# Optimization experiments

Hardware: AMD Instinct MI355X
Metric: run time of the kernel (lower is better)

Reference implementation:

```python
import jax, jax.numpy as jnp
import numpy as np

COST_CLASS, COST_BBOX, COST_GIOU = 2.0, 5.0, 2.0
ALPHA, GAMMA, EPS = 0.25, 2.0, 1e-8


def _cxcywh_to_xyxy(b):
    cx, cy, w, h = b[..., 0], b[..., 1], b[..., 2], b[..., 3]
    return jnp.stack([cx - 0.5 * w, cy - 0.5 * h, cx + 0.5 * w, cy + 0.5 * h], axis=-1)


def _generalized_box_iou(boxes1, boxes2):
    # boxes1: [N,4], boxes2: [T,4] in xyxy -> [N,T]
    area1 = (boxes1[:, 2] - boxes1[:, 0]) * (boxes1[:, 3] - boxes1[:, 1])
    area2 = (boxes2[:, 2] - boxes2[:, 0]) * (boxes2[:, 3] - boxes2[:, 1])
    lt = jnp.maximum(boxes1[:, None, :2], boxes2[None, :, :2])
    rb = jnp.minimum(boxes1[:, None, 2:], boxes2[None, :, 2:])
    wh = jnp.clip(rb - lt, 0.0)
    inter = wh[..., 0] * wh[..., 1]
    union = area1[:, None] + area2[None, :] - inter
    iou = inter / union
    lt_e = jnp.minimum(boxes1[:, None, :2], boxes2[None, :, :2])
    rb_e = jnp.maximum(boxes1[:, None, 2:], boxes2[None, :, 2:])
    wh_e = jnp.clip(rb_e - lt_e, 0.0)
    area_e = wh_e[..., 0] * wh_e[..., 1]
    return iou - (area_e - union) / area_e


def setup_inputs() -> dict:
    key = jax.random.key(0)
    k1, k2, k3, k4 = jax.random.split(key, 4)
    bs, nq, nc, T = 16, 900, 91, 1600
    pred_logits = jax.random.normal(k1, (bs, nq, nc), dtype=jnp.float32)
    pred_boxes = jax.random.uniform(k2, (bs, nq, 4), dtype=jnp.float32)
    tgt_ids = jax.random.randint(k3, (T,), 0, nc, dtype=jnp.int64) if jax.config.jax_enable_x64 else jax.random.randint(k3, (T,), 0, nc, dtype=jnp.int32)
    tgt_bbox = jax.random.uniform(k4, (T, 4), dtype=jnp.float32)
    return {"pred_logits": pred_logits, "pred_boxes": pred_boxes,
            "tgt_ids": tgt_ids, "tgt_bbox": tgt_bbox}


def reference(pred_logits, pred_boxes, tgt_ids, tgt_bbox):
    bs, nq, nc = pred_logits.shape
    out_prob = jax.nn.sigmoid(pred_logits.reshape(bs * nq, nc))  # [N, C]
    out_bbox = pred_boxes.reshape(bs * nq, 4)                    # [N, 4]

    # -GIoU cost
    cost_giou = -_generalized_box_iou(_cxcywh_to_xyxy(out_bbox), _cxcywh_to_xyxy(tgt_bbox))

    # focal-style classification cost (alpha/gamma hardcoded in the source forward)
    neg_cost_class = (1.0 - ALPHA) * out_prob ** GAMMA * (-jnp.log(1.0 - out_prob + EPS))
    pos_cost_class = ALPHA * (1.0 - out_prob) ** GAMMA * (-jnp.log(out_prob + EPS))
    cost_class = pos_cost_class[:, tgt_ids] - neg_cost_class[:, tgt_ids]  # [N, T]

    # L1 cdist between box vectors
    cost_bbox = jnp.sum(jnp.abs(out_bbox[:, None, :] - tgt_bbox[None, :, :]), axis=-1)

    C = COST_BBOX * cost_bbox + COST_CLASS * cost_class + COST_GIOU * cost_giou
    return C.reshape(bs, nq, -1)
```

## Files before the change

### kernel.cpp

```cpp
#include <hip/hip_runtime.h>


#define NC 91
#define TT 1600
#define T4 (TT / 4)
#define ROWS 16
#define RPAD 20
#define NTHREADS 448
#define TABN (ROWS * NC)
#define TAB4 (TABN / 4)

typedef float vfloat4 __attribute__((ext_vector_type(4)));

__device__ __forceinline__ float focal_tab(float x) {
    const float p = __builtin_amdgcn_rcpf(1.f + __expf(-x));
    const float omp = 1.f - p;
    const float neg = 0.75f * p * p * (-__logf(omp + 1e-8f));
    const float pos = 0.25f * omp * omp * (-__logf(p + 1e-8f));
    return 2.f * (pos - neg) + 2.f;
}

__global__ __launch_bounds__(NTHREADS, 4) void matcher_kernel(
    const float* __restrict__ logits,
    const float4* __restrict__ pboxes,
    const int4* __restrict__ tids,
    const float4* __restrict__ tboxes,
    vfloat4* __restrict__ out)
{
    __shared__ __align__(16) float tab_t[NC * RPAD];

    const int n0 = blockIdx.x * ROWS;
    const int tid = threadIdx.x;
    const bool active = (tid < T4);

    int4 ids = {0, 0, 0, 0};
    float4 tb[4];
    if (active) {
        ids = tids[tid];
#pragma unroll
        for (int j = 0; j < 4; ++j) tb[j] = tboxes[tid * 4 + j];
    }

    if (tid < TAB4) {
        const float4 v = *reinterpret_cast<const float4*>(
            logits + (size_t)n0 * NC + 4 * (size_t)tid);
        const float vv[4] = {v.x, v.y, v.z, v.w};
#pragma unroll
        for (int k = 0; k < 4; ++k) {
            const int e = 4 * tid + k;
            const int r = e / NC;
            const int c = e - r * NC;
            tab_t[c * RPAD + r] = focal_tab(vv[k]);
        }
    }
    __syncthreads();

    if (!active) return;

    const int idv[4] = {ids.x, ids.y, ids.z, ids.w};
    float tx0[4], ty0[4], tx1[4], ty1[4];
#pragma unroll
    for (int j = 0; j < 4; ++j) {
        tx0[j] = tb[j].x - 0.5f * tb[j].z;
        ty0[j] = tb[j].y - 0.5f * tb[j].w;
        tx1[j] = tb[j].x + 0.5f * tb[j].z;
        ty1[j] = tb[j].y + 0.5f * tb[j].w;
    }

    vfloat4 tv[4][4];
#pragma unroll
    for (int j = 0; j < 4; ++j) {
#pragma unroll
        for (int q = 0; q < 4; ++q)
            tv[j][q] = *reinterpret_cast<const vfloat4*>(
                &tab_t[idv[j] * RPAD + 4 * q]);
    }

#pragma unroll
    for (int r = 0; r < ROWS; ++r) {
        const float4 b = pboxes[n0 + r];
        const float pcx = b.x, pcy = b.y, pw = b.z, ph = b.w;
        const float px0 = pcx - 0.5f * pw, py0 = pcy - 0.5f * ph;
        const float px1 = pcx + 0.5f * pw, py1 = pcy + 0.5f * ph;
        const float pa  = pw * ph;
        vfloat4 res;
#pragma unroll
        for (int j = 0; j < 4; ++j) {
            const float tw = tx1[j] - tx0[j];
            const float th = ty1[j] - ty0[j];
            const float iwr = fminf(px1, tx1[j]) - fmaxf(px0, tx0[j]);
            const float ihr = fminf(py1, ty1[j]) - fmaxf(py0, ty0[j]);
            const float inter = fmaxf(iwr, 0.f) * fmaxf(ihr, 0.f);
            const float uni = pa + tw * th - inter;
            const float ew = (pw + tw) - iwr;
            const float eh = (ph + th) - ihr;
            const float ae = ew * eh;
            const float tcx = tx0[j] + 0.5f * tw;
            const float tcy = ty0[j] + 0.5f * th;
            const float l1 = fabsf(pcx - tcx) + fabsf(pcy - tcy)
                           + fabsf(pw - tw) + fabsf(ph - th);
            res[j] = 5.f * l1 + tv[j][r >> 2][r & 3]
                   - 2.f * inter * __builtin_amdgcn_rcpf(uni)
                   - 2.f * uni * __builtin_amdgcn_rcpf(ae);
        }
        out[(size_t)(n0 + r) * T4 + tid] = res;
    }
}

extern "C" void kernel_launch(void* const* d_in, const int* in_sizes, int n_in,
                              void* d_out, int out_size, void* d_ws, size_t ws_size,
                              hipStream_t stream) {
    const float* logits  = (const float*)d_in[0];
    const float4* pboxes = (const float4*)d_in[1];
    const int4* tids     = (const int4*)d_in[2];
    const float4* tboxes = (const float4*)d_in[3];
    vfloat4* out = (vfloat4*)d_out;
    const int N = in_sizes[1] / 4;
    matcher_kernel<<<N / ROWS, NTHREADS, 0, stream>>>(logits, pboxes, tids, tboxes, out);
}
```

Before: 120.5 us.

## Make matcher kernel persistent over two row groups with double-buffered focal table

```diff
diff --git a/kernel.cpp b/kernel.cpp
--- a/kernel.cpp
+++ b/kernel.cpp
@@ -20,18 +20,30 @@
     return 2.f * (pos - neg) + 2.f;
 }
 
+__device__ __forceinline__ void focal_to_tab(float* tabbuf, int tid, float4 v) {
+    const float vv[4] = {v.x, v.y, v.z, v.w};
+#pragma unroll
+    for (int k = 0; k < 4; ++k) {
+        const int e = 4 * tid + k;
+        const int r = e / NC;
+        const int c = e - r * NC;
+        tabbuf[c * RPAD + r] = focal_tab(vv[k]);
+    }
+}
+
 __global__ __launch_bounds__(NTHREADS, 4) void matcher_kernel(
     const float* __restrict__ logits,
     const float4* __restrict__ pboxes,
     const int4* __restrict__ tids,
     const float4* __restrict__ tboxes,
-    vfloat4* __restrict__ out)
+    vfloat4* __restrict__ out,
+    int ngroups)
 {
-    __shared__ __align__(16) float tab_t[NC * RPAD];
+    __shared__ __align__(16) float tab[2][NC * RPAD];
 
-    const int n0 = blockIdx.x * ROWS;
     const int tid = threadIdx.x;
     const bool active = (tid < T4);
+    const bool ftab = (tid < TAB4);
 
     int4 ids = {0, 0, 0, 0};
     float4 tb[4];
@@ -41,21 +53,11 @@
         for (int j = 0; j < 4; ++j) tb[j] = tboxes[tid * 4 + j];
     }
 
-    if (tid < TAB4) {
-        const float4 v = *reinterpret_cast<const float4*>(
-            logits + (size_t)n0 * NC + 4 * (size_t)tid);
-        const float vv[4] = {v.x, v.y, v.z, v.w};
-#pragma unroll
-        for (int k = 0; k < 4; ++k) {
-            const int e = 4 * tid + k;
-            const int r = e / NC;
-            const int c = e - r * NC;
-            tab_t[c * RPAD + r] = focal_tab(vv[k]);
-        }
-    }
-    __syncthreads();
-
-    if (!active) return;
+    const int g0 = blockIdx.x;
+    float4 lg;
+    if (ftab)
+        lg = *reinterpret_cast<const float4*>(
+            logits + (size_t)g0 * ROWS * NC + 4 * (size_t)tid);
 
     const int idv[4] = {ids.x, ids.y, ids.z, ids.w};
     float tx0[4], ty0[4], tx1[4], ty1[4];
@@ -67,43 +69,61 @@
         ty1[j] = tb[j].y + 0.5f * tb[j].w;
     }
 
-    vfloat4 tv[4][4];
+    if (ftab) focal_to_tab(tab[0], tid, lg);
+
+    int buf = 0;
+    for (int g = g0; g < ngroups; g += gridDim.x) {
+        __syncthreads();
+
+        const int gn = g + gridDim.x;
+        float4 lgn;
+        if (gn < ngroups && ftab)
+            lgn = *reinterpret_cast<const float4*>(
+                logits + (size_t)gn * ROWS * NC + 4 * (size_t)tid);
+
+        if (active) {
+            vfloat4 tv[4][4];
 #pragma unroll
-    for (int j = 0; j < 4; ++j) {
+            for (int j = 0; j < 4; ++j)
 #pragma unroll
-        for (int q = 0; q < 4; ++q)
-            tv[j][q] = *reinterpret_cast<const vfloat4*>(
-                &tab_t[idv[j] * RPAD + 4 * q]);
-    }
+                for (int q = 0; q < 4; ++q)
+                    tv[j][q] = *reinterpret_cast<const vfloat4*>(
+                        &tab[buf][idv[j] * RPAD + 4 * q]);
 
+            const int n0 = g * ROWS;
 #pragma unroll
-    for (int r = 0; r < ROWS; ++r) {
-        const float4 b = pboxes[n0 + r];
-        const float pcx = b.x, pcy = b.y, pw = b.z, ph = b.w;
-        const float px0 = pcx - 0.5f * pw, py0 = pcy - 0.5f * ph;
-        const float px1 = pcx + 0.5f * pw, py1 = pcy + 0.5f * ph;
-        const float pa  = pw * ph;
-        vfloat4 res;
+            for (int r = 0; r < ROWS; ++r) {
+                const float4 b = pboxes[n0 + r];
+                const float pcx = b.x, pcy = b.y, pw = b.z, ph = b.w;
+                const float px0 = pcx - 0.5f * pw, py0 = pcy - 0.5f * ph;
+                const float px1 = pcx + 0.5f * pw, py1 = pcy + 0.5f * ph;
+                const float pa  = pw * ph;
+                vfloat4 res;
 #pragma unroll
-        for (int j = 0; j < 4; ++j) {
-            const float tw = tx1[j] - tx0[j];
-            const float th = ty1[j] - ty0[j];
-            const float iwr = fminf(px1, tx1[j]) - fmaxf(px0, tx0[j]);
-            const float ihr = fminf(py1, ty1[j]) - fmaxf(py0, ty0[j]);
-            const float inter = fmaxf(iwr, 0.f) * fmaxf(ihr, 0.f);
-            const float uni = pa + tw * th - inter;
-            const float ew = (pw + tw) - iwr;
-            const float eh = (ph + th) - ihr;
-            const float ae = ew * eh;
-            const float tcx = tx0[j] + 0.5f * tw;
-            const float tcy = ty0[j] + 0.5f * th;
-            const float l1 = fabsf(pcx - tcx) + fabsf(pcy - tcy)
-                           + fabsf(pw - tw) + fabsf(ph - th);
-            res[j] = 5.f * l1 + tv[j][r >> 2][r & 3]
-                   - 2.f * inter * __builtin_amdgcn_rcpf(uni)
-                   - 2.f * uni * __builtin_amdgcn_rcpf(ae);
+                for (int j = 0; j < 4; ++j) {
+                    const float tw = tx1[j] - tx0[j];
+                    const float th = ty1[j] - ty0[j];
+                    const float iwr = fminf(px1, tx1[j]) - fmaxf(px0, tx0[j]);
+                    const float ihr = fminf(py1, ty1[j]) - fmaxf(py0, ty0[j]);
+                    const float inter = fmaxf(iwr, 0.f) * fmaxf(ihr, 0.f);
+                    const float uni = pa + tw * th - inter;
+                    const float ew = (pw + tw) - iwr;
+                    const float eh = (ph + th) - ihr;
+                    const float ae = ew * eh;
+                    const float tcx = tx0[j] + 0.5f * tw;
+                    const float tcy = ty0[j] + 0.5f * th;
+                    const float l1 = fabsf(pcx - tcx) + fabsf(pcy - tcy)
+                                   + fabsf(pw - tw) + fabsf(ph - th);
+                    res[j] = 5.f * l1 + tv[j][r >> 2][r & 3]
+                           - 2.f * inter * __builtin_amdgcn_rcpf(uni)
+                           - 2.f * uni * __builtin_amdgcn_rcpf(ae);
+                }
+                out[(size_t)(n0 + r) * T4 + tid] = res;
+            }
         }
-        out[(size_t)(n0 + r) * T4 + tid] = res;
+
+        if (gn < ngroups && ftab) focal_to_tab(tab[buf ^ 1], tid, lgn);
+        buf ^= 1;
     }
 }
 
@@ -116,5 +136,8 @@
     const float4* tboxes = (const float4*)d_in[3];
     vfloat4* out = (vfloat4*)d_out;
     const int N = in_sizes[1] / 4;
-    matcher_kernel<<<N / ROWS, NTHREADS, 0, stream>>>(logits, pboxes, tids, tboxes, out);
+    const int ngroups = N / ROWS;
+    const int nblocks = (ngroups + 1) / 2;
+    matcher_kernel<<<nblocks, NTHREADS, 0, stream>>>(logits, pboxes, tids,
+                                                     tboxes, out, ngroups);
 }
```

Measured after the change: 124.0 us. 1.03x slower.
